# Optimization experiments

Hardware: AMD Instinct MI355X
Metric: run time of the kernel (lower is better)

## Reference

```python
import jax, jax.numpy as jnp
import numpy as np

B, D, S = 16, 64, 2048


def setup_inputs() -> dict:
    key = jax.random.key(0)
    kq, kk, kv, km = jax.random.split(key, 4)
    q = jax.random.normal(kq, (B, D, S), dtype=jnp.float32)
    k = jax.random.normal(kk, (B, D, S), dtype=jnp.float32)
    v = jax.random.normal(kv, (B, D, S), dtype=jnp.float32)
    # boolean mask over the [B, Sq, Sk] score matrix (True -> filled with -1000)
    mask = jax.random.bernoulli(km, 0.1, (B, S, S))
    return {"q": q, "k": k, "v": v, "mask": mask}


def reference(q, k, v, mask):
    dim = jnp.asarray(D, dtype=q.dtype)
    # scores[b, s, t] = sum_d q[b, d, s] * k[b, d, t] / sqrt(D)
    scores = jnp.einsum("bds,bdt->bst", q, k) / jnp.sqrt(dim)
    scores = jnp.where(mask, jnp.asarray(-1000.0, dtype=scores.dtype), scores)
    # NOTE: softmax over dim=1 (the QUERY axis), faithful to nn.Softmax(dim=1)
    attn = jax.nn.softmax(scores, axis=1)
    # out[b, s, d] = sum_t attn[b, s, t] * v[b, d, t]
    out = jnp.einsum("bst,bdt->bsd", attn, v)
    return out
```

## Files before the change

### kernel.cpp

```cpp
#include <hip/hip_runtime.h>
#include <hip/hip_bf16.h>
#include <stdint.h>


namespace {
constexpr int B = 16;
constexpr int D = 64;
constexpr int S = 2048;
constexpr float SCALE = 0.125f;

typedef __attribute__((ext_vector_type(8))) short short8;
typedef __attribute__((ext_vector_type(4))) float f32x4;

constexpr size_t WS_FLAG  = 0;
constexpr size_t WS_LINV  = 256;
constexpr size_t WS_LPART = 256 + 131072;
constexpr size_t WS_QT    = 655616;
constexpr size_t WS_KT    = 4849920;
constexpr size_t WS_VB    = 9044224;
constexpr size_t WS_MPACK = 13238528;
constexpr size_t NEED_OLD = 13238528;
constexpr size_t NEED_T1  = 21627136;
}

__device__ __forceinline__ bool mask_at(const void* mask, int mode, size_t idx) {
    if (mode == 1) return ((const int*)mask)[idx] != 0;
    if (mode == 2) return ((const float*)mask)[idx] != 0.0f;
    return ((const unsigned char*)mask)[idx] != 0;
}

__device__ __forceinline__ uint16_t f2bf(float f) {
    unsigned int u = __float_as_uint(f);
    unsigned int r = (u + 0x7fffu + ((u >> 16) & 1u)) >> 16;
    return (uint16_t)r;
}
__device__ __forceinline__ unsigned int pack2(float a, float b) {
    return (unsigned int)f2bf(a) | ((unsigned int)f2bf(b) << 16);
}

__device__ __forceinline__ int swz(int row, int colByte) {
    return row * 128 + (colByte ^ ((row & 7) << 4));
}

__device__ __forceinline__ void gll16(const void* g, void* l) {
    __builtin_amdgcn_global_load_lds(
        (const __attribute__((address_space(1))) void*)g,
        (__attribute__((address_space(3))) void*)l, 16, 0, 0);
}

__device__ __forceinline__ void stage_tile(const char* srcRows, size_t rowStrideB,
                                           unsigned char* dst, int tid) {
    const int lane = tid & 63, w = tid >> 6;
    const int lrow = lane >> 3;
    const int slot = (lane & 7) ^ lrow;
    #pragma unroll
    for (int c = 0; c < 2; ++c) {
        const int row = 16 * w + 8 * c + lrow;
        gll16(srcRows + (size_t)row * rowStrideB + slot * 16,
              dst + (16 * w + 8 * c) * 128);
    }
}

__device__ __forceinline__ void stage_tile32(const char* srcRows, size_t rowStrideB,
                                             unsigned char* dst, int tid) {
    const int lane = tid & 63, w = tid >> 6;
    const int lrow = lane >> 3;
    const int slot = (lane & 7) ^ lrow;
    const int row = 8 * w + lrow;
    gll16(srcRows + (size_t)row * rowStrideB + slot * 16, dst + 8 * w * 128);
}

__device__ __forceinline__ f32x4 mfma16(short8 a, short8 b, f32x4 c) {
    return __builtin_amdgcn_mfma_f32_16x16x32_bf16(a, b, c, 0, 0, 0);
}

__device__ __forceinline__ void probe_body(const unsigned char* mask, int* flag,
                                           int tid, int* c0s, int* c123s) {
    if (tid == 0) { *c0s = 0; *c123s = 0; }
    __syncthreads();
    int c0 = 0, c123 = 0;
    for (int f = tid; f < 65536; f += 256) {
        const int nz = (mask[f] != 0) ? 1 : 0;
        if ((f & 3) == 0) c0 += nz; else c123 += nz;
    }
    atomicAdd(c0s, c0);
    atomicAdd(c123s, c123);
    __syncthreads();
    if (tid == 0) {
        int mode = 0;
        if (*c123s == 0) mode = 1;
        else if (*c0s == 0) mode = 2;
        *flag = mode;
    }
}

__global__ void probe_mask_kernel(const unsigned char* __restrict__ mask,
                                  int* __restrict__ flag)
{
    __shared__ int c0s, c123s;
    probe_body(mask, flag, threadIdx.x, &c0s, &c123s);
}

__global__ __launch_bounds__(256, 2)
void prep_kernel(const float* __restrict__ q, const float* __restrict__ k,
                 const float* __restrict__ v,
                 uint16_t* __restrict__ qT, uint16_t* __restrict__ kT,
                 uint16_t* __restrict__ vb,
                 const unsigned char* __restrict__ mask, int* __restrict__ flag)
{
    __shared__ float ts[64][65];
    const int tid = threadIdx.x;
    const int s0 = blockIdx.x * 64;
    const int b  = blockIdx.y;

    if (blockIdx.z == 2) {
        const int d = tid >> 2, c = tid & 3;
        const float* row = v + ((size_t)b * D + d) * S + s0 + c * 16;
        uint16_t*   orow = vb + ((size_t)b * D + d) * S + s0 + c * 16;
        #pragma unroll
        for (int i = 0; i < 4; ++i) {
            float4 v4 = *(const float4*)(row + 4 * i);
            uint16_t t4[4] = {f2bf(v4.x), f2bf(v4.y), f2bf(v4.z), f2bf(v4.w)};
            *(uint2*)(orow + 4 * i) = *(const uint2*)t4;
        }
        if (blockIdx.x == 0 && blockIdx.y == 0) {
            __shared__ int c0s, c123s;
            probe_body(mask, flag, tid, &c0s, &c123s);
        }
        return;
    }

    const float* src = blockIdx.z ? k : q;
    uint16_t*    dst = blockIdx.z ? kT : qT;
    {
        const int d = tid >> 2, c = tid & 3;
        const float* row = src + ((size_t)b * D + d) * S + s0 + c * 16;
        #pragma unroll
        for (int i = 0; i < 4; ++i) {
            float4 v4 = *(const float4*)(row + 4 * i);
            ts[c * 16 + 4 * i + 0][d] = v4.x;
            ts[c * 16 + 4 * i + 1][d] = v4.y;
            ts[c * 16 + 4 * i + 2][d] = v4.z;
            ts[c * 16 + 4 * i + 3][d] = v4.w;
        }
    }
    __syncthreads();
    {
        const int srow = tid >> 2, p = tid & 3;
        uint16_t tmp[16];
        #pragma unroll
        for (int j = 0; j < 16; ++j) tmp[j] = f2bf(ts[srow][p * 16 + j]);
        uint16_t* drow = dst + ((size_t)b * S + s0 + srow) * 64 + p * 16;
        *(uint4*)drow       = ((const uint4*)tmp)[0];
        *((uint4*)drow + 1) = ((const uint4*)tmp)[1];
    }
}

__global__ __launch_bounds__(256, 4)
void pass1_kernel(const uint16_t* __restrict__ qT, const uint16_t* __restrict__ kT,
                  const void* __restrict__ mask, const int* __restrict__ flagp,
                  float* __restrict__ lpart, unsigned long long* __restrict__ mpackT)
{
    __shared__ __align__(16) unsigned char ksb[64 * 128];
    __shared__ __align__(16) unsigned char qsb[64 * 128];
    __shared__ unsigned short mbits[64][4];
    __shared__ float red[4][64];

    const int tid = threadIdx.x;
    const int lane = tid & 63, w = tid >> 6;
    const int l = lane & 15, hh = lane >> 4;
    const int t0 = blockIdx.x * 64;
    const int chunk = blockIdx.y;
    const int b = blockIdx.z;
    const int mode = *flagp;

    const int row_m = tid >> 2, cq = tid & 3;
    const size_t mrow_base = ((size_t)b * S + row_m) * S + t0 + cq * 16;

    int4  mr4[4];
    uint4 mr1;
    auto load_mtile = [&](int sbase) {
        if (mode != 0) {
            const int4* p = (const int4*)((const int*)mask + mrow_base + (size_t)sbase * S);
            mr4[0] = p[0]; mr4[1] = p[1]; mr4[2] = p[2]; mr4[3] = p[3];
        } else {
            mr1 = *(const uint4*)((const unsigned char*)mask + mrow_base + (size_t)sbase * S);
        }
    };
    auto pack_mtile = [&]() -> unsigned int {
        unsigned int bits = 0;
        if (mode != 0) {
            #pragma unroll
            for (int i = 0; i < 4; ++i) {
                bits |= (mr4[i].x ? 1u : 0u) << (4 * i + 0);
                bits |= (mr4[i].y ? 1u : 0u) << (4 * i + 1);
                bits |= (mr4[i].z ? 1u : 0u) << (4 * i + 2);
                bits |= (mr4[i].w ? 1u : 0u) << (4 * i + 3);
            }
        } else {
            const unsigned int u[4] = {mr1.x, mr1.y, mr1.z, mr1.w};
            #pragma unroll
            for (int c = 0; c < 4; ++c) {
                bits |= ((u[c] & 0x000000FFu) ? 1u : 0u) << (4 * c + 0);
                bits |= ((u[c] & 0x0000FF00u) ? 1u : 0u) << (4 * c + 1);
                bits |= ((u[c] & 0x00FF0000u) ? 1u : 0u) << (4 * c + 2);
                bits |= ((u[c] & 0xFF000000u) ? 1u : 0u) << (4 * c + 3);
            }
        }
        return bits;
    };

    stage_tile((const char*)(kT + ((size_t)b * S + t0) * 64), 128, ksb, tid);
    stage_tile((const char*)(qT + ((size_t)b * S + chunk * 512) * 64), 128, qsb, tid);
    load_mtile(chunk * 512);

    float colacc[4] = {0.f, 0.f, 0.f, 0.f};

    for (int it = 0; it < 8; ++it) {
        const int sbase = chunk * 512 + it * 64;

        __syncthreads();

        const unsigned int bits = pack_mtile();
        mbits[row_m][cq] = (unsigned short)bits;

        short8 A0 = *(const short8*)&qsb[swz(16 * w + l, 0  + hh * 16)];
        short8 A1 = *(const short8*)&qsb[swz(16 * w + l, 64 + hh * 16)];

        __syncthreads();

        if (tid < 64) {
            const unsigned long long word =
                (unsigned long long)mbits[tid][0]
                | ((unsigned long long)mbits[tid][1] << 16)
                | ((unsigned long long)mbits[tid][2] << 32)
                | ((unsigned long long)mbits[tid][3] << 48);
            mpackT[((size_t)b * 32 + (t0 >> 6)) * S + sbase + tid] = word;
        }

        if (it < 7) {
            stage_tile((const char*)(qT + ((size_t)b * S + sbase + 64) * 64), 128, qsb, tid);
            load_mtile(sbase + 64);
        }

        const int srow_l = 16 * w + 4 * hh;
        #pragma unroll
        for (int tf = 0; tf < 4; ++tf) {
            const short8 B0 = *(const short8*)&ksb[swz(tf * 16 + l, 0  + hh * 16)];
            const short8 B1 = *(const short8*)&ksb[swz(tf * 16 + l, 64 + hh * 16)];
            f32x4 c4 = {0.f, 0.f, 0.f, 0.f};
            c4 = mfma16(A0, B0, c4);
            c4 = mfma16(A1, B1, c4);
            #pragma unroll
            for (int r = 0; r < 4; ++r) {
                if (!((mbits[srow_l + r][tf] >> l) & 1))
                    colacc[tf] += __expf(c4[r] * SCALE);
            }
        }
    }

    #pragma unroll
    for (int tf = 0; tf < 4; ++tf) {
        colacc[tf] += __shfl_xor(colacc[tf], 16);
        colacc[tf] += __shfl_xor(colacc[tf], 32);
    }
    __syncthreads();
    if (lane < 16) {
        #pragma unroll
        for (int tf = 0; tf < 4; ++tf) red[w][tf * 16 + lane] = colacc[tf];
    }
    __syncthreads();
    if (tid < 64) {
        const float s = red[0][tid] + red[1][tid] + red[2][tid] + red[3][tid];
        lpart[(size_t)chunk * (B * S) + (size_t)b * S + t0 + tid] = s;
    }
}

__global__ __launch_bounds__(256, 4)
void pass2_kernel(const uint16_t* __restrict__ qT, const uint16_t* __restrict__ kT,
                  const uint16_t* __restrict__ vb,
                  const unsigned long long* __restrict__ mpackT,
                  const float* __restrict__ lpart, float* __restrict__ out)
{
    __shared__ __align__(16) unsigned char qsb[32 * 128];
    __shared__ __align__(16) unsigned char ksb[64 * 128];
    __shared__ __align__(16) unsigned char vsb[64 * 128];
    __shared__ __align__(16) unsigned char ptb[32 * 128];
    __shared__ unsigned long long mrow2[2][32];
    __shared__ float linv_s[2][64];

    const int tid = threadIdx.x;
    const int lane = tid & 63, w = tid >> 6;
    const int l = lane & 15, hh = lane >> 4;
    const int s0 = blockIdx.x * 32;
    const int b = blockIdx.y;

    auto load_meta = [&](int tile, int slot) {
        if (tid < 64) {
            const int t = tile * 64 + tid;
            const float s = lpart[(size_t)b * S + t]
                          + lpart[(size_t)(B * S) + b * S + t]
                          + lpart[(size_t)(2 * B * S) + b * S + t]
                          + lpart[(size_t)(3 * B * S) + b * S + t];
            linv_s[slot][tid] = 1.0f / s;
        } else if (tid < 96) {
            mrow2[slot][tid - 64] =
                mpackT[((size_t)b * 32 + tile) * S + s0 + (tid - 64)];
        }
    };

    stage_tile32((const char*)(qT + ((size_t)b * S + s0) * 64), 128, qsb, tid);
    stage_tile((const char*)(kT + (size_t)b * S * 64), 128, ksb, tid);
    stage_tile((const char*)(vb + (size_t)b * D * S), (size_t)S * 2, vsb, tid);
    load_meta(0, 0);
    __syncthreads();

    short8 QB[2][2];
    #pragma unroll
    for (int sf = 0; sf < 2; ++sf)
        #pragma unroll
        for (int kh = 0; kh < 2; ++kh)
            QB[sf][kh] = *(const short8*)&qsb[swz(sf * 16 + l, kh * 64 + hh * 16)];

    f32x4 oacc[2];
    oacc[0] = (f32x4){0.f, 0.f, 0.f, 0.f};
    oacc[1] = (f32x4){0.f, 0.f, 0.f, 0.f};

    const int sb = w & 1;
    const int dh = w >> 1;

    for (int i = 0; i < 32; ++i) {
        const int cur = i & 1, nxt = cur ^ 1;

        if (i > 0)
            stage_tile((const char*)(vb + (size_t)b * D * S + i * 64),
                       (size_t)S * 2, vsb, tid);

        short8 KA0 = *(const short8*)&ksb[swz(16 * w + l, 0  + hh * 16)];
        short8 KA1 = *(const short8*)&ksb[swz(16 * w + l, 64 + hh * 16)];
        float lv[4];
        #pragma unroll
        for (int r = 0; r < 4; ++r) lv[r] = linv_s[cur][16 * w + 4 * hh + r];

        #pragma unroll
        for (int sf = 0; sf < 2; ++sf) {
            f32x4 c4 = {0.f, 0.f, 0.f, 0.f};
            c4 = mfma16(KA0, QB[sf][0], c4);
            c4 = mfma16(KA1, QB[sf][1], c4);
            const unsigned long long bits = mrow2[cur][sf * 16 + l];
            float pv[4];
            #pragma unroll
            for (int r = 0; r < 4; ++r) {
                const int tloc = 16 * w + 4 * hh + r;
                pv[r] = ((bits >> tloc) & 1ull) ? 0.f : __expf(c4[r] * SCALE) * lv[r];
            }
            const int row = sf * 16 + l;
            const int cb = (32 * w + 8 * hh);
            *(uint2*)&ptb[row * 128 + (cb ^ ((row & 7) << 4))] =
                make_uint2(pack2(pv[0], pv[1]), pack2(pv[2], pv[3]));
        }
        __syncthreads();

        if (i + 1 < 32) {
            stage_tile((const char*)(kT + ((size_t)b * S + (i + 1) * 64) * 64),
                       128, ksb, tid);
            load_meta(i + 1, nxt);
        }

        short8 PA0 = *(const short8*)&ptb[swz(sb * 16 + l, 0  + hh * 16)];
        short8 PA1 = *(const short8*)&ptb[swz(sb * 16 + l, 64 + hh * 16)];
        #pragma unroll
        for (int df = 0; df < 2; ++df) {
            const int drow = (dh * 2 + df) * 16 + l;
            short8 VB0 = *(const short8*)&vsb[swz(drow, 0  + hh * 16)];
            short8 VB1 = *(const short8*)&vsb[swz(drow, 64 + hh * 16)];
            oacc[df] = mfma16(PA0, VB0, oacc[df]);
            oacc[df] = mfma16(PA1, VB1, oacc[df]);
        }
        __syncthreads();
    }

    #pragma unroll
    for (int df = 0; df < 2; ++df)
        #pragma unroll
        for (int r = 0; r < 4; ++r)
            out[((size_t)b * S + s0 + sb * 16 + 4 * hh + r) * D
                + (dh * 2 + df) * 16 + l] = oacc[df][r];
}

__global__ __launch_bounds__(256, 2)
void transpose_cvt_kernel(const float* __restrict__ q, const float* __restrict__ k,
                          uint16_t* __restrict__ qT, uint16_t* __restrict__ kT)
{
    __shared__ float ts[64][65];
    const int tid = threadIdx.x;
    const int s0 = blockIdx.x * 64;
    const int b  = blockIdx.y;
    const float* src = blockIdx.z ? k : q;
    uint16_t*    dst = blockIdx.z ? kT : qT;
    {
        const int d = tid >> 2, c = tid & 3;
        const float* row = src + ((size_t)b * D + d) * S + s0 + c * 16;
        #pragma unroll
        for (int i = 0; i < 4; ++i) {
            float4 v4 = *(const float4*)(row + 4 * i);
            ts[c * 16 + 4 * i + 0][d] = v4.x;
            ts[c * 16 + 4 * i + 1][d] = v4.y;
            ts[c * 16 + 4 * i + 2][d] = v4.z;
            ts[c * 16 + 4 * i + 3][d] = v4.w;
        }
    }
    __syncthreads();
    {
        const int srow = tid >> 2, p = tid & 3;
        uint16_t tmp[16];
        #pragma unroll
        for (int j = 0; j < 16; ++j) tmp[j] = f2bf(ts[srow][p * 16 + j]);
        uint16_t* drow = dst + ((size_t)b * S + s0 + srow) * 64 + p * 16;
        *(uint4*)drow       = ((const uint4*)tmp)[0];
        *((uint4*)drow + 1) = ((const uint4*)tmp)[1];
    }
}

__global__ void cvt_v_kernel(const float* __restrict__ v, uint16_t* __restrict__ vb)
{
    const size_t i = ((size_t)blockIdx.x * 256 + threadIdx.x) * 4;
    float4 v4 = *(const float4*)(v + i);
    uint16_t t4[4] = {f2bf(v4.x), f2bf(v4.y), f2bf(v4.z), f2bf(v4.w)};
    *(uint2*)(vb + i) = *(const uint2*)t4;
}

__global__ void linv_kernel(const float* __restrict__ lpart, float* __restrict__ linv)
{
    const int i = blockIdx.x * 256 + threadIdx.x;
    const float s = lpart[i] + lpart[B * S + i] + lpart[2 * B * S + i] + lpart[3 * B * S + i];
    linv[i] = 1.0f / s;
}

__global__ __launch_bounds__(256, 2)
void pass1_old_kernel(const uint16_t* __restrict__ qT, const uint16_t* __restrict__ kT,
                      const void* __restrict__ mask, const int* __restrict__ flagp,
                      float* __restrict__ lpart)
{
    __shared__ __align__(16) unsigned char ksb[64 * 128];
    __shared__ __align__(16) unsigned char qsb[64 * 128];
    __shared__ float red[4][64];
    const int tid = threadIdx.x;
    const int lane = tid & 63, w = tid >> 6;
    const int l = lane & 15, hh = lane >> 4;
    const int t0 = blockIdx.x * 64;
    const int chunk = blockIdx.y;
    const int b = blockIdx.z;
    const int mode = *flagp;
    const size_t mbase = (size_t)b * S * S;

    stage_tile((const char*)(kT + ((size_t)b * S + t0) * 64), 128, ksb, tid);
    __syncthreads();
    short8 BF[4][2];
    #pragma unroll
    for (int tf = 0; tf < 4; ++tf)
        #pragma unroll
        for (int kh = 0; kh < 2; ++kh)
            BF[tf][kh] = *(const short8*)&ksb[swz(tf * 16 + l, kh * 64 + hh * 16)];
    float colacc[4] = {0.f, 0.f, 0.f, 0.f};
    for (int it = 0; it < 8; ++it) {
        const int sbase = chunk * 512 + it * 64;
        __syncthreads();
        stage_tile((const char*)(qT + ((size_t)b * S + sbase) * 64), 128, qsb, tid);
        __syncthreads();
        short8 A0 = *(const short8*)&qsb[swz(16 * w + l, 0  + hh * 16)];
        short8 A1 = *(const short8*)&qsb[swz(16 * w + l, 64 + hh * 16)];
        #pragma unroll
        for (int tf = 0; tf < 4; ++tf) {
            f32x4 c4 = {0.f, 0.f, 0.f, 0.f};
            c4 = mfma16(A0, BF[tf][0], c4);
            c4 = mfma16(A1, BF[tf][1], c4);
            const int t = t0 + tf * 16 + l;
            const int srow = sbase + 16 * w + 4 * hh;
            #pragma unroll
            for (int r = 0; r < 4; ++r)
                if (!mask_at(mask, mode, mbase + (size_t)(srow + r) * S + t))
                    colacc[tf] += __expf(c4[r] * SCALE);
        }
    }
    #pragma unroll
    for (int tf = 0; tf < 4; ++tf) {
        colacc[tf] += __shfl_xor(colacc[tf], 16);
        colacc[tf] += __shfl_xor(colacc[tf], 32);
    }
    if (lane < 16) {
        #pragma unroll
        for (int tf = 0; tf < 4; ++tf) red[w][tf * 16 + lane] = colacc[tf];
    }
    __syncthreads();
    if (tid < 64) {
        const float s = red[0][tid] + red[1][tid] + red[2][tid] + red[3][tid];
        lpart[(size_t)chunk * (B * S) + (size_t)b * S + t0 + tid] = s;
    }
}

__global__ __launch_bounds__(256, 2)
void pass2_old_kernel(const uint16_t* __restrict__ qT, const uint16_t* __restrict__ kT,
                      const uint16_t* __restrict__ vb, const void* __restrict__ mask,
                      const int* __restrict__ flagp, const float* __restrict__ linv,
                      float* __restrict__ out)
{
    __shared__ __align__(16) unsigned char qsb[64 * 128];
    __shared__ __align__(16) unsigned char ksb[64 * 128];
    __shared__ __align__(16) unsigned char vsb[64 * 128];
    __shared__ __align__(16) unsigned char ptb[64 * 128];
    __shared__ unsigned short mbits[64][4];
    __shared__ float linv_s[64];
    const int tid = threadIdx.x;
    const int lane = tid & 63, w = tid >> 6;
    const int l = lane & 15, hh = lane >> 4;
    const int s0 = blockIdx.x * 64;
    const int b = blockIdx.y;
    const int mode = *flagp;
    const size_t mbase = (size_t)b * S * S;

    stage_tile((const char*)(qT + ((size_t)b * S + s0) * 64), 128, qsb, tid);
    __syncthreads();
    short8 QB[4][2];
    #pragma unroll
    for (int sf = 0; sf < 4; ++sf)
        #pragma unroll
        for (int kh = 0; kh < 2; ++kh)
            QB[sf][kh] = *(const short8*)&qsb[swz(sf * 16 + l, kh * 64 + hh * 16)];
    f32x4 oacc[4];
    #pragma unroll
    for (int df = 0; df < 4; ++df) oacc[df] = (f32x4){0.f, 0.f, 0.f, 0.f};

    for (int t0 = 0; t0 < S; t0 += 64) {
        stage_tile((const char*)(kT + ((size_t)b * S + t0) * 64), 128, ksb, tid);
        stage_tile((const char*)(vb + (size_t)b * D * S + t0), (size_t)S * 2, vsb, tid);
        {
            const int srow = tid >> 2, c = tid & 3;
            const size_t base = mbase + (size_t)(s0 + srow) * S + t0 + c * 16;
            unsigned int bits = 0;
            #pragma unroll
            for (int j = 0; j < 16; ++j)
                bits |= (mask_at(mask, mode, base + j) ? 1u : 0u) << j;
            mbits[srow][c] = (unsigned short)bits;
        }
        if (tid < 64) linv_s[tid] = linv[(size_t)b * S + t0 + tid];
        __syncthreads();

        short8 KA0 = *(const short8*)&ksb[swz(16 * w + l, 0  + hh * 16)];
        short8 KA1 = *(const short8*)&ksb[swz(16 * w + l, 64 + hh * 16)];
        float lv[4];
        #pragma unroll
        for (int r = 0; r < 4; ++r) lv[r] = linv_s[16 * w + 4 * hh + r];
        #pragma unroll
        for (int sf = 0; sf < 4; ++sf) {
            f32x4 c4 = {0.f, 0.f, 0.f, 0.f};
            c4 = mfma16(KA0, QB[sf][0], c4);
            c4 = mfma16(KA1, QB[sf][1], c4);
            const unsigned int mb = (unsigned int)mbits[sf * 16 + l][w] >> (4 * hh);
            float pv[4];
            #pragma unroll
            for (int r = 0; r < 4; ++r)
                pv[r] = ((mb >> r) & 1u) ? 0.f : __expf(c4[r] * SCALE) * lv[r];
            const int row = sf * 16 + l;
            const int cb = (32 * w + 8 * hh);
            *(uint2*)&ptb[row * 128 + (cb ^ ((row & 7) << 4))] =
                make_uint2(pack2(pv[0], pv[1]), pack2(pv[2], pv[3]));
        }
        __syncthreads();
        short8 PA0 = *(const short8*)&ptb[swz(16 * w + l, 0  + hh * 16)];
        short8 PA1 = *(const short8*)&ptb[swz(16 * w + l, 64 + hh * 16)];
        #pragma unroll
        for (int df = 0; df < 4; ++df) {
            short8 VB0 = *(const short8*)&vsb[swz(df * 16 + l, 0  + hh * 16)];
            short8 VB1 = *(const short8*)&vsb[swz(df * 16 + l, 64 + hh * 16)];
            oacc[df] = mfma16(PA0, VB0, oacc[df]);
            oacc[df] = mfma16(PA1, VB1, oacc[df]);
        }
        __syncthreads();
    }
    #pragma unroll
    for (int df = 0; df < 4; ++df)
        #pragma unroll
        for (int r = 0; r < 4; ++r)
            out[((size_t)b * S + s0 + 16 * w + 4 * hh + r) * D + df * 16 + l] = oacc[df][r];
}

__global__ __launch_bounds__(256, 2)
void colsum_fb(const float* __restrict__ q, const float* __restrict__ k,
               const void* __restrict__ mask, const int* __restrict__ flagp,
               float* __restrict__ lsums)
{
    __shared__ __align__(16) float qs[128][68];
    __shared__ __align__(16) float ks[64][68];
    __shared__ float lred[32][66];
    const int tid = threadIdx.x;
    const int b = blockIdx.y;
    const int t0 = blockIdx.x * 64;
    const int mode = *flagp;
    {
        const int tl = tid & 63, d0 = tid >> 6;
        #pragma unroll
        for (int i = 0; i < 16; ++i) { const int d = d0 + i * 4; ks[tl][d] = k[(b * D + d) * S + t0 + tl]; }
    }
    const int tq = tid & 7, sq = tid >> 3;
    float lacc[8];
    #pragma unroll
    for (int j = 0; j < 8; ++j) lacc[j] = 0.f;
    const size_t mbase = (size_t)b * S * S;
    for (int s0 = 0; s0 < S; s0 += 128) {
        __syncthreads();
        {
            const int sl = tid & 127, d0 = tid >> 7;
            #pragma unroll
            for (int i = 0; i < 32; ++i) { const int d = d0 + i * 2; qs[sl][d] = q[(b * D + d) * S + s0 + sl]; }
        }
        __syncthreads();
        float acc[4][8];
        #pragma unroll
        for (int jj = 0; jj < 4; ++jj)
            #pragma unroll
            for (int j = 0; j < 8; ++j) acc[jj][j] = 0.f;
        #pragma unroll
        for (int dblk = 0; dblk < 16; ++dblk) {
            float4 q4[4];
            #pragma unroll
            for (int jj = 0; jj < 4; ++jj) q4[jj] = *(const float4*)&qs[sq + 32 * jj][dblk * 4];
            #pragma unroll
            for (int j = 0; j < 8; ++j) {
                const float4 k4 = *(const float4*)&ks[tq + 8 * j][dblk * 4];
                #pragma unroll
                for (int jj = 0; jj < 4; ++jj)
                    acc[jj][j] += q4[jj].x * k4.x + q4[jj].y * k4.y + q4[jj].z * k4.z + q4[jj].w * k4.w;
            }
        }
        #pragma unroll
        for (int jj = 0; jj < 4; ++jj) {
            const int sg = s0 + sq + 32 * jj;
            const size_t ridx = mbase + (size_t)sg * S + t0;
            #pragma unroll
            for (int j = 0; j < 8; ++j)
                if (!mask_at(mask, mode, ridx + tq + 8 * j)) lacc[j] += __expf(acc[jj][j] * SCALE);
        }
    }
    __syncthreads();
    #pragma unroll
    for (int j = 0; j < 8; ++j) lred[sq][tq + 8 * j] = lacc[j];
    __syncthreads();
    if (tid < 64) {
        float s = 0.f;
        #pragma unroll
        for (int i = 0; i < 32; ++i) s += lred[i][tid];
        lsums[b * S + t0 + tid] = s;
    }
}

__global__ __launch_bounds__(256, 2)
void attn_out_fb(const float* __restrict__ q, const float* __restrict__ k,
                 const float* __restrict__ v, const void* __restrict__ mask,
                 const int* __restrict__ flagp, const float* __restrict__ lsums,
                 float* __restrict__ out)
{
    __shared__ __align__(16) float qs[64][68];
    __shared__ __align__(16) float kw[64][68];
    __shared__ __align__(16) float pt[64][68];
    __shared__ float linv_sh[64];
    const int tid = threadIdx.x;
    const int b = blockIdx.y;
    const int s0 = blockIdx.x * 64;
    const int mode = *flagp;
    {
        const int sl = tid & 63, d0 = tid >> 6;
        #pragma unroll
        for (int i = 0; i < 16; ++i) { const int d = d0 + i * 4; qs[sl][d] = q[(b * D + d) * S + s0 + sl]; }
    }
    const int tq = tid & 7, sq = tid >> 3;
    float oacc[2][8];
    #pragma unroll
    for (int jj = 0; jj < 2; ++jj)
        #pragma unroll
        for (int dd = 0; dd < 8; ++dd) oacc[jj][dd] = 0.f;
    const size_t mbase = (size_t)b * S * S;
    for (int t0 = 0; t0 < S; t0 += 64) {
        __syncthreads();
        if (tid < 64) linv_sh[tid] = 1.f / lsums[b * S + t0 + tid];
        {
            const int tl = tid & 63, d0 = tid >> 6;
            #pragma unroll
            for (int i = 0; i < 16; ++i) { const int d = d0 + i * 4; kw[tl][d] = k[(b * D + d) * S + t0 + tl]; }
        }
        __syncthreads();
        float sc[2][8];
        #pragma unroll
        for (int jj = 0; jj < 2; ++jj)
            #pragma unroll
            for (int j = 0; j < 8; ++j) sc[jj][j] = 0.f;
        #pragma unroll
        for (int dblk = 0; dblk < 16; ++dblk) {
            float4 q4[2];
            #pragma unroll
            for (int jj = 0; jj < 2; ++jj) q4[jj] = *(const float4*)&qs[sq + 32 * jj][dblk * 4];
            #pragma unroll
            for (int j = 0; j < 8; ++j) {
                const float4 k4 = *(const float4*)&kw[tq + 8 * j][dblk * 4];
                #pragma unroll
                for (int jj = 0; jj < 2; ++jj)
                    sc[jj][j] += q4[jj].x * k4.x + q4[jj].y * k4.y + q4[jj].z * k4.z + q4[jj].w * k4.w;
            }
        }
        #pragma unroll
        for (int jj = 0; jj < 2; ++jj) {
            const int sg = s0 + sq + 32 * jj;
            const size_t ridx = mbase + (size_t)sg * S + t0;
            #pragma unroll
            for (int j = 0; j < 8; ++j) {
                const int tl = tq + 8 * j;
                const bool msk = mask_at(mask, mode, ridx + tl);
                pt[tl][sq + 32 * jj] = msk ? 0.f : __expf(sc[jj][j] * SCALE) * linv_sh[tl];
            }
        }
        __syncthreads();
        {
            const int tl = tid & 63, d0 = tid >> 6;
            #pragma unroll
            for (int i = 0; i < 16; ++i) { const int d = d0 + i * 4; kw[tl][d] = v[(b * D + d) * S + t0 + tl]; }
        }
        __syncthreads();
        #pragma unroll 8
        for (int t = 0; t < 64; ++t) {
            const float2 p2 = *(const float2*)&pt[t][sq * 2];
            const float4 w0 = *(const float4*)&kw[t][tq * 8];
            const float4 w1 = *(const float4*)&kw[t][tq * 8 + 4];
            oacc[0][0] += p2.x * w0.x; oacc[0][1] += p2.x * w0.y; oacc[0][2] += p2.x * w0.z; oacc[0][3] += p2.x * w0.w;
            oacc[0][4] += p2.x * w1.x; oacc[0][5] += p2.x * w1.y; oacc[0][6] += p2.x * w1.z; oacc[0][7] += p2.x * w1.w;
            oacc[1][0] += p2.y * w0.x; oacc[1][1] += p2.y * w0.y; oacc[1][2] += p2.y * w0.z; oacc[1][3] += p2.y * w0.w;
            oacc[1][4] += p2.y * w1.x; oacc[1][5] += p2.y * w1.y; oacc[1][6] += p2.y * w1.z; oacc[1][7] += p2.y * w1.w;
        }
    }
    #pragma unroll
    for (int jj = 0; jj < 2; ++jj) {
        float* dst = out + ((size_t)(b * S + s0 + sq * 2 + jj)) * D + tq * 8;
        *(float4*)dst = make_float4(oacc[jj][0], oacc[jj][1], oacc[jj][2], oacc[jj][3]);
        *(float4*)(dst + 4) = make_float4(oacc[jj][4], oacc[jj][5], oacc[jj][6], oacc[jj][7]);
    }
}

extern "C" void kernel_launch(void* const* d_in, const int* in_sizes, int n_in,
                              void* d_out, int out_size, void* d_ws, size_t ws_size,
                              hipStream_t stream) {
    const float* q = (const float*)d_in[0];
    const float* k = (const float*)d_in[1];
    const float* v = (const float*)d_in[2];
    const void*  mask = d_in[3];
    float* out = (float*)d_out;
    char* ws = (char*)d_ws;

    int* flag = (int*)(ws + WS_FLAG);

    if (ws_size >= NEED_T1) {
        float*    lpart = (float*)(ws + WS_LPART);
        uint16_t* qT    = (uint16_t*)(ws + WS_QT);
        uint16_t* kT    = (uint16_t*)(ws + WS_KT);
        uint16_t* vb    = (uint16_t*)(ws + WS_VB);
        unsigned long long* mpackT = (unsigned long long*)(ws + WS_MPACK);

        prep_kernel<<<dim3(S / 64, B, 3), 256, 0, stream>>>(
            q, k, v, qT, kT, vb, (const unsigned char*)mask, flag);
        pass1_kernel<<<dim3(S / 64, 4, B), 256, 0, stream>>>(
            qT, kT, mask, flag, lpart, mpackT);
        pass2_kernel<<<dim3(S / 32, B), 256, 0, stream>>>(
            qT, kT, vb, mpackT, lpart, out);
    } else if (ws_size >= NEED_OLD) {
        float*    linv  = (float*)(ws + WS_LINV);
        float*    lpart = (float*)(ws + WS_LPART);
        uint16_t* qT    = (uint16_t*)(ws + WS_QT);
        uint16_t* kT    = (uint16_t*)(ws + WS_KT);
        uint16_t* vb    = (uint16_t*)(ws + WS_VB);
        probe_mask_kernel<<<1, 256, 0, stream>>>((const unsigned char*)mask, flag);
        transpose_cvt_kernel<<<dim3(S / 64, B, 2), 256, 0, stream>>>(q, k, qT, kT);
        cvt_v_kernel<<<(B * D * S) / (256 * 4), 256, 0, stream>>>(v, vb);
        pass1_old_kernel<<<dim3(S / 64, 4, B), 256, 0, stream>>>(qT, kT, mask, flag, lpart);
        linv_kernel<<<(B * S) / 256, 256, 0, stream>>>(lpart, linv);
        pass2_old_kernel<<<dim3(S / 64, B), 256, 0, stream>>>(qT, kT, vb, mask, flag, linv, out);
    } else {
        float* lsums = (float*)(ws + WS_LINV);
        probe_mask_kernel<<<1, 256, 0, stream>>>((const unsigned char*)mask, flag);
        dim3 grid(S / 64, B);
        colsum_fb<<<grid, 256, 0, stream>>>(q, k, mask, flag, lsums);
        attn_out_fb<<<grid, 256, 0, stream>>>(q, k, v, mask, flag, lsums, out);
    }
}
```

Baseline: 169.4 us.

## Double-buffer Q tile and mask bits to drop per-iteration block barriers in pass1

The Q staging buffer and the packed mask-bit array in pass1 become two-slot ping-pong buffers. The two __syncthreads per loop iteration are replaced by a vmcnt wait plus a scheduling barrier. The next Q tile and mask tile are issued before the current MFMA work. This relies on each wave only touching its own 16 rows of Q and mask bits, so waves can run without block-wide barriers. It doubles that part of LDS and would race if staging ever crossed wave boundaries.

Result: no change. 171.3 us (+1.1%).

```diff
diff --git a/kernel.cpp b/kernel.cpp
--- a/kernel.cpp
+++ b/kernel.cpp
@@ -162,8 +162,8 @@
                   float* __restrict__ lpart, unsigned long long* __restrict__ mpackT)
 {
     __shared__ __align__(16) unsigned char ksb[64 * 128];
-    __shared__ __align__(16) unsigned char qsb[64 * 128];
-    __shared__ unsigned short mbits[64][4];
+    __shared__ __align__(16) unsigned char qsb[2][64 * 128];
+    __shared__ unsigned short mbits[2][64][4];
     __shared__ float red[4][64];
 
     const int tid = threadIdx.x;
@@ -173,6 +173,7 @@
     const int chunk = blockIdx.y;
     const int b = blockIdx.z;
     const int mode = *flagp;
+    const bool wide = (mode != 0);
 
     const int row_m = tid >> 2, cq = tid & 3;
     const size_t mrow_base = ((size_t)b * S + row_m) * S + t0 + cq * 16;
@@ -180,7 +181,7 @@
     int4  mr4[4];
     uint4 mr1;
     auto load_mtile = [&](int sbase) {
-        if (mode != 0) {
+        if (wide) {
             const int4* p = (const int4*)((const int*)mask + mrow_base + (size_t)sbase * S);
             mr4[0] = p[0]; mr4[1] = p[1]; mr4[2] = p[2]; mr4[3] = p[3];
         } else {
@@ -189,7 +190,7 @@
     };
     auto pack_mtile = [&]() -> unsigned int {
         unsigned int bits = 0;
-        if (mode != 0) {
+        if (wide) {
             #pragma unroll
             for (int i = 0; i < 4; ++i) {
                 bits |= (mr4[i].x ? 1u : 0u) << (4 * i + 0);
@@ -211,39 +212,43 @@
     };
 
     stage_tile((const char*)(kT + ((size_t)b * S + t0) * 64), 128, ksb, tid);
-    stage_tile((const char*)(qT + ((size_t)b * S + chunk * 512) * 64), 128, qsb, tid);
+    stage_tile((const char*)(qT + ((size_t)b * S + chunk * 512) * 64), 128, qsb[0], tid);
     load_mtile(chunk * 512);
+    __syncthreads();
 
     float colacc[4] = {0.f, 0.f, 0.f, 0.f};
+    const int srow_l = 16 * w + 4 * hh;
+    const size_t mpk_base = ((size_t)b * 32 + (t0 >> 6)) * S;
 
     for (int it = 0; it < 8; ++it) {
+        const int buf = it & 1;
         const int sbase = chunk * 512 + it * 64;
 
-        __syncthreads();
+        asm volatile("s_waitcnt vmcnt(0)" ::: "memory");
+        __builtin_amdgcn_sched_barrier(0);
 
         const unsigned int bits = pack_mtile();
-        mbits[row_m][cq] = (unsigned short)bits;
-
-        short8 A0 = *(const short8*)&qsb[swz(16 * w + l, 0  + hh * 16)];
-        short8 A1 = *(const short8*)&qsb[swz(16 * w + l, 64 + hh * 16)];
-
-        __syncthreads();
-
-        if (tid < 64) {
+        mbits[buf][row_m][cq] = (unsigned short)bits;
+
+        if (it < 7) {
+            stage_tile((const char*)(qT + ((size_t)b * S + sbase + 64) * 64), 128,
+                       qsb[buf ^ 1], tid);
+            load_mtile(sbase + 64);
+        }
+
+        short8 A0 = *(const short8*)&qsb[buf][swz(16 * w + l, 0  + hh * 16)];
+        short8 A1 = *(const short8*)&qsb[buf][swz(16 * w + l, 64 + hh * 16)];
+
+        if (lane < 16) {
+            const int rr = 16 * w + lane;
             const unsigned long long word =
-                (unsigned long long)mbits[tid][0]
-                | ((unsigned long long)mbits[tid][1] << 16)
-                | ((unsigned long long)mbits[tid][2] << 32)
-                | ((unsigned long long)mbits[tid][3] << 48);
-            mpackT[((size_t)b * 32 + (t0 >> 6)) * S + sbase + tid] = word;
-        }
-
-        if (it < 7) {
-            stage_tile((const char*)(qT + ((size_t)b * S + sbase + 64) * 64), 128, qsb, tid);
-            load_mtile(sbase + 64);
-        }
-
-        const int srow_l = 16 * w + 4 * hh;
+                (unsigned long long)mbits[buf][rr][0]
+                | ((unsigned long long)mbits[buf][rr][1] << 16)
+                | ((unsigned long long)mbits[buf][rr][2] << 32)
+                | ((unsigned long long)mbits[buf][rr][3] << 48);
+            mpackT[mpk_base + sbase + rr] = word;
+        }
+
         #pragma unroll
         for (int tf = 0; tf < 4; ++tf) {
             const short8 B0 = *(const short8*)&ksb[swz(tf * 16 + l, 0  + hh * 16)];
@@ -253,7 +258,7 @@
             c4 = mfma16(A1, B1, c4);
             #pragma unroll
             for (int r = 0; r < 4; ++r) {
-                if (!((mbits[srow_l + r][tf] >> l) & 1))
+                if (!((mbits[buf][srow_l + r][tf] >> l) & 1))
                     colacc[tf] += __expf(c4[r] * SCALE);
             }
         }
```
